# Kernel optimization log

Measured on AMD Instinct MI355X. Metric: run time of the kernel, lower is better.

Reference implementation:

```python
import jax, jax.numpy as jnp
import numpy as np

B, N, D, H = 32, 4096, 768, 384

def setup_inputs() -> dict:
    key = jax.random.key(0)
    k1, k2, k3 = jax.random.split(key, 3)
    patch_tokens = jax.random.normal(k1, (B, N, D), dtype=jnp.float32)
    # score head params (kaiming-like scale)
    w1 = jax.random.normal(k2, (D, H), dtype=jnp.float32) * (2.0 / H) ** 0.5
    b1 = jnp.zeros((H,), dtype=jnp.float32)
    w2 = jax.random.normal(k3, (H,), dtype=jnp.float32) * (2.0 / 1) ** 0.5
    b2 = jnp.zeros((), dtype=jnp.float32)
    return {"patch_tokens": patch_tokens, "w1": w1, "b1": b1, "w2": w2, "b2": b2,
            "keep_ratio_pct": 50}

def reference(patch_tokens, w1, b1, w2, b2, keep_ratio_pct):
    # score head: Linear -> GELU (erf variant, torch default) -> Linear(->1)
    h = jax.nn.gelu(jnp.einsum('bnd,dh->bnh', patch_tokens, w1) + b1, approximate=False)
    patch_logits = jnp.einsum('bnh,h->bn', h, w2) + b2                 # [B, N]
    foreground_scores = jax.nn.sigmoid(patch_logits)                    # [B, N]

    patch_count = patch_tokens.shape[1]
    keep_count = max(1, int(patch_count * keep_ratio_pct / 100))
    keep_count = min(keep_count, patch_count)

    if keep_count == patch_count:
        keep_mask = jnp.ones_like(foreground_scores)
    else:
        topk_scores, _ = jax.lax.top_k(foreground_scores, keep_count)   # [B, k], sorted desc
        keep_threshold = jax.lax.stop_gradient(topk_scores[:, -1:])     # [B, 1]
        keep_mask = (foreground_scores >= keep_threshold).astype(foreground_scores.dtype)

    filtered_scores = foreground_scores * keep_mask
    filtered_weights = filtered_scores / (jnp.sum(filtered_scores, axis=1, keepdims=True) + 1e-12)
    filtered_feat = jnp.einsum('bn,bnd->bd', filtered_weights, patch_tokens)  # [B, D]
    return (filtered_feat, filtered_weights, foreground_scores, keep_mask)
```

## Files before the change

kernel.cpp:

```cpp
#include <hip/hip_runtime.h>
#include <math.h>

#define BB 32
#define NN 4096
#define DD 768
#define HH 384
#define NCH 8

typedef _Float16 half8 __attribute__((ext_vector_type(8)));
typedef float f32x4 __attribute__((ext_vector_type(4)));

__global__ __launch_bounds__(64) void fapf_prep_w(
    const float* __restrict__ w1, short* __restrict__ whf, short* __restrict__ wlf)
{
    const int cf = blockIdx.x;
    const int kg = blockIdx.y;
    const int l  = threadIdx.x;
    const int c  = cf * 16 + (l & 15);
    const int kb = kg * 32 + (l >> 4) * 8;

    short hs[8], ls[8];
#pragma unroll
    for (int i = 0; i < 8; i++) {
        float v = w1[(size_t)(kb + i) * HH + c];
        _Float16 hi = (_Float16)v;
        _Float16 lo = (_Float16)(v - (float)hi);
        hs[i] = *(short*)&hi;
        ls[i] = *(short*)&lo;
    }
    size_t base = ((size_t)(kg * 24 + cf) * 64 + l) * 8;
#pragma unroll
    for (int i = 0; i < 8; i++) { whf[base + i] = hs[i]; wlf[base + i] = ls[i]; }
}

__global__ __launch_bounds__(256)
__attribute__((amdgpu_waves_per_eu(3)))
void fapf_scores_mfma(
    const float* __restrict__ x, const short* __restrict__ whf,
    const short* __restrict__ wlf, const float* __restrict__ b1,
    const float* __restrict__ w2, const float* __restrict__ b2,
    float* __restrict__ scores)
{
    __shared__ __align__(16) short xh[2][32 * 64];
    __shared__ __align__(16) short xl[2][32 * 64];
    __shared__ float part[32][4];

    const int tid = threadIdx.x;
    const int l   = tid & 63;
    const int cw  = tid >> 6;
    const int t0  = blockIdx.x * 32;

    f32x4 acc[2][6];
#pragma unroll
    for (int fr = 0; fr < 2; fr++)
#pragma unroll
        for (int cf = 0; cf < 6; cf++) acc[fr][cf] = (f32x4){0.f, 0.f, 0.f, 0.f};

    const half8* whp = (const half8*)whf + (size_t)(cw * 6) * 64 + l;
    const half8* wlp = (const half8*)wlf + (size_t)(cw * 6) * 64 + l;

    float4 xv[2];

#define LOADX(ch)                                                            \
    {                                                                        \
        _Pragma("unroll")                                                    \
        for (int it = 0; it < 2; it++) {                                     \
            int id = it * 256 + tid;                                         \
            xv[it] = *(const float4*)&x[(size_t)(t0 + (id >> 4)) * DD        \
                                        + (ch) * 64 + (id & 15) * 4];        \
        }                                                                    \
    }

#define SPLITWRITE(buf)                                                      \
    {                                                                        \
        _Pragma("unroll")                                                    \
        for (int it = 0; it < 2; it++) {                                     \
            int id = it * 256 + tid;                                         \
            int row = id >> 4, seg = id & 15;                                \
            union { short s[4]; uint2 u; } ph, pl;                           \
            float vv[4] = {xv[it].x, xv[it].y, xv[it].z, xv[it].w};          \
            _Pragma("unroll")                                                \
            for (int i = 0; i < 4; i++) {                                    \
                _Float16 hi = (_Float16)vv[i];                               \
                _Float16 lo = (_Float16)(vv[i] - (float)hi);                 \
                ph.s[i] = *(short*)&hi;                                      \
                pl.s[i] = *(short*)&lo;                                      \
            }                                                                \
            int idx = (row * 64 + seg * 4) ^ ((row & 7) << 3);               \
            *(uint2*)&xh[buf][idx] = ph.u;                                   \
            *(uint2*)&xl[buf][idx] = pl.u;                                   \
        }                                                                    \
    }

#define LOADB(dst, ptr, kg)                                                  \
    {                                                                        \
        _Pragma("unroll")                                                    \
        for (int cf = 0; cf < 6; cf++)                                       \
            dst[cf] = (ptr)[(size_t)(kg) * 1536 + (size_t)cf * 64];          \
    }

    LOADX(0);
    SPLITWRITE(0);
    half8 bA[6], bB[6];
    LOADB(bA, whp, 0);
    __syncthreads();

    for (int c = 0; c < 12; c++) {
        const int cur = c & 1;

#pragma unroll
        for (int ks = 0; ks < 2; ks++) {
            const int kg = c * 2 + ks;

            half8 ah[2], al[2];
#pragma unroll
            for (int fr = 0; fr < 2; fr++) {
                int row = fr * 16 + (l & 15);
                int idx = (row * 64 + ks * 32 + (l >> 4) * 8) ^ ((row & 7) << 3);
                ah[fr] = *(const half8*)&xh[cur][idx];
                al[fr] = *(const half8*)&xl[cur][idx];
            }

            LOADB(bB, wlp, kg);

            __builtin_amdgcn_s_setprio(1);
#pragma unroll
            for (int fr = 0; fr < 2; fr++)
#pragma unroll
                for (int cf = 0; cf < 6; cf++)
                    acc[fr][cf] = __builtin_amdgcn_mfma_f32_16x16x32_f16(
                        ah[fr], bA[cf], acc[fr][cf], 0, 0, 0);
#pragma unroll
            for (int fr = 0; fr < 2; fr++)
#pragma unroll
                for (int cf = 0; cf < 6; cf++)
                    acc[fr][cf] = __builtin_amdgcn_mfma_f32_16x16x32_f16(
                        al[fr], bA[cf], acc[fr][cf], 0, 0, 0);
            __builtin_amdgcn_s_setprio(0);

            if (kg < 23) LOADB(bA, whp, kg + 1);

            if (ks == 0 && c < 11) LOADX(c + 1);

            __builtin_amdgcn_s_setprio(1);
#pragma unroll
            for (int fr = 0; fr < 2; fr++)
#pragma unroll
                for (int cf = 0; cf < 6; cf++)
                    acc[fr][cf] = __builtin_amdgcn_mfma_f32_16x16x32_f16(
                        ah[fr], bB[cf], acc[fr][cf], 0, 0, 0);
            __builtin_amdgcn_s_setprio(0);
        }

        if (c < 11) {
            SPLITWRITE(cur ^ 1);
            __syncthreads();
        }
    }

    float b1v[6], w2v[6];
#pragma unroll
    for (int cf = 0; cf < 6; cf++) {
        int col = cw * 96 + cf * 16 + (l & 15);
        b1v[cf] = b1[col];
        w2v[cf] = w2[col];
    }
    float p[2][4];
#pragma unroll
    for (int fr = 0; fr < 2; fr++)
#pragma unroll
        for (int j = 0; j < 4; j++) p[fr][j] = 0.f;
#pragma unroll
    for (int fr = 0; fr < 2; fr++)
#pragma unroll
        for (int cf = 0; cf < 6; cf++)
#pragma unroll
            for (int j = 0; j < 4; j++) {
                float hh = acc[fr][cf][j] + b1v[cf];
                float g  = 0.5f * hh * (1.f + erff(hh * 0.70710678118654752f));
                p[fr][j] = fmaf(g, w2v[cf], p[fr][j]);
            }
#pragma unroll
    for (int m = 8; m >= 1; m >>= 1)
#pragma unroll
        for (int fr = 0; fr < 2; fr++)
#pragma unroll
            for (int j = 0; j < 4; j++)
                p[fr][j] += __shfl_xor(p[fr][j], m, 64);

    if ((l & 15) == 0) {
#pragma unroll
        for (int fr = 0; fr < 2; fr++)
#pragma unroll
            for (int j = 0; j < 4; j++) {
                int row = fr * 16 + (l >> 4) * 4 + j;
                part[row][cw] = p[fr][j];
            }
    }
    __syncthreads();
    if (tid < 32) {
        float lg = part[tid][0] + part[tid][1] + part[tid][2] + part[tid][3] + b2[0];
        scores[t0 + tid] = 1.f / (1.f + expf(-lg));
    }
#undef LOADX
#undef SPLITWRITE
#undef LOADB
}

__global__ __launch_bounds__(1024) void fapf_select_kernel(
    const float* __restrict__ scores, const int* __restrict__ pct_p,
    float* __restrict__ weights, float* __restrict__ mask,
    float* __restrict__ feat, int* __restrict__ kidx,
    float* __restrict__ kw, int* __restrict__ kcnt)
{
    __shared__ float s[NN];
    __shared__ float red[1024];
    __shared__ int scnt;
    const int b = blockIdx.x, tid = threadIdx.x;

    if (tid == 0) scnt = 0;
    for (int i = tid; i < DD; i += 1024) feat[b * DD + i] = 0.f;
    for (int i = tid; i < NN; i += 1024) s[i] = scores[b * NN + i];
    __syncthreads();

    for (int k = 2; k <= NN; k <<= 1) {
        for (int j = k >> 1; j > 0; j >>= 1) {
            for (int i = tid; i < NN; i += 1024) {
                int ixj = i ^ j;
                if (ixj > i) {
                    bool up = ((i & k) == 0);
                    float a = s[i], c = s[ixj];
                    if (up ? (a > c) : (a < c)) { s[i] = c; s[ixj] = a; }
                }
            }
            __syncthreads();
        }
    }

    int pct = pct_p[0];
    long long kcl = (long long)NN * pct / 100;
    int kc = (int)kcl;
    if (kc < 1) kc = 1;
    if (kc > NN) kc = NN;
    float thr = s[NN - kc];

    float local = 0.f;
    for (int i = tid; i < NN; i += 1024) {
        float v = scores[b * NN + i];
        if (v >= thr) local += v;
    }
    red[tid] = local;
    __syncthreads();
    for (int step = 512; step > 0; step >>= 1) {
        if (tid < step) red[tid] += red[tid + step];
        __syncthreads();
    }
    float inv = 1.f / (red[0] + 1e-12f);
    const int lane = tid & 63;
    for (int i = tid; i < NN; i += 1024) {
        float v = scores[b * NN + i];
        bool keep = (v >= thr);
        float m = keep ? 1.f : 0.f;
        weights[b * NN + i] = v * m * inv;
        mask[b * NN + i]    = m;
        if (kidx) {
            unsigned long long bal = __ballot(keep);
            int base = 0;
            if (lane == 0) base = atomicAdd(&scnt, __popcll(bal));
            base = __shfl(base, 0, 64);
            if (keep) {
                int off = __popcll(bal & ((1ULL << lane) - 1ULL));
                kidx[b * NN + base + off] = i;
                kw[b * NN + base + off]   = v * inv;
            }
        }
    }
    if (kidx) {
        __syncthreads();
        if (tid == 0) kcnt[b] = scnt;
    }
}

__global__ __launch_bounds__(256) void fapf_feat_compact(
    const float* __restrict__ x, const int* __restrict__ kidx,
    const float* __restrict__ kw, const int* __restrict__ kcnt,
    float* __restrict__ feat)
{
    const int b  = blockIdx.y;
    const int d0 = blockIdx.x * 64;
    const int ch = blockIdx.z;
    const int dl = threadIdx.x & 63;
    const int ng = threadIdx.x >> 6;

    const int cnt = kcnt[b];
    int per = (cnt + NCH - 1) / NCH;
    int j0 = ch * per; if (j0 > cnt) j0 = cnt;
    int j1 = j0 + per; if (j1 > cnt) j1 = cnt;
    int len = j1 - j0;
    int per_w = (len + 3) >> 2;
    int s = j0 + ng * per_w;
    int e = s + per_w; if (e > j1) e = j1;

    const float* xb  = x + (size_t)b * NN * DD + d0 + dl;
    const int*   ib  = kidx + b * NN;
    const float* wbp = kw + b * NN;

    float a[8];
#pragma unroll
    for (int u = 0; u < 8; u++) a[u] = 0.f;

    int j = s;
    for (; j + 8 <= e; j += 8) {
        int   idx[8];
        float ww[8];
#pragma unroll
        for (int u = 0; u < 8; u++) { idx[u] = ib[j + u]; ww[u] = wbp[j + u]; }
#pragma unroll
        for (int u = 0; u < 8; u++)
            a[u] = fmaf(ww[u], xb[(size_t)idx[u] * DD], a[u]);
    }
    for (; j < e; j++)
        a[0] = fmaf(wbp[j], xb[(size_t)ib[j] * DD], a[0]);

    float acc = ((a[0] + a[1]) + (a[2] + a[3])) + ((a[4] + a[5]) + (a[6] + a[7]));

    __shared__ float red[4][64];
    red[ng][dl] = acc;
    __syncthreads();
    if (threadIdx.x < 64) {
        float v = (red[0][dl] + red[1][dl]) + (red[2][dl] + red[3][dl]);
        atomicAdd(&feat[b * DD + d0 + dl], v);
    }
}

__global__ __launch_bounds__(256) void fapf_feat_dense(
    const float* __restrict__ x, const float* __restrict__ weights,
    float* __restrict__ feat)
{
    const int b  = blockIdx.y;
    const int d0 = blockIdx.x * 64;
    const int dl = threadIdx.x & 63;
    const int ng = threadIdx.x >> 6;

    const float* xb = x + (size_t)b * NN * DD;
    const float* wb = weights + b * NN;

    float a0 = 0.f, a1 = 0.f, a2 = 0.f, a3 = 0.f;
    for (int n = ng; n < NN; n += 16) {
        float w0 = wb[n], w1v = wb[n + 4], w2v = wb[n + 8], w3 = wb[n + 12];
        float v0 = xb[(size_t)(n)      * DD + d0 + dl];
        float v1 = xb[(size_t)(n + 4)  * DD + d0 + dl];
        float v2 = xb[(size_t)(n + 8)  * DD + d0 + dl];
        float v3 = xb[(size_t)(n + 12) * DD + d0 + dl];
        a0 = fmaf(w0, v0, a0);
        a1 = fmaf(w1v, v1, a1);
        a2 = fmaf(w2v, v2, a2);
        a3 = fmaf(w3, v3, a3);
    }
    float acc = (a0 + a1) + (a2 + a3);

    __shared__ float red[4][64];
    red[ng][dl] = acc;
    __syncthreads();
    if (threadIdx.x < 64) {
        feat[b * DD + d0 + dl] =
            (red[0][dl] + red[1][dl]) + (red[2][dl] + red[3][dl]);
    }
}

extern "C" void kernel_launch(void* const* d_in, const int* in_sizes, int n_in,
                              void* d_out, int out_size, void* d_ws, size_t ws_size,
                              hipStream_t stream) {
    const float* x   = (const float*)d_in[0];
    const float* w1  = (const float*)d_in[1];
    const float* b1  = (const float*)d_in[2];
    const float* w2  = (const float*)d_in[3];
    const float* b2  = (const float*)d_in[4];
    const int*   pct = (const int*)d_in[5];

    float* out = (float*)d_out;
    float* feat    = out;
    float* weights = out + BB * DD;
    float* scores  = weights + BB * NN;
    float* mask    = scores + BB * NN;

    short* whf  = (short*)d_ws;
    short* wlf  = whf + 24 * 24 * 64 * 8;
    int*   kidx = (int*)(wlf + 24 * 24 * 64 * 8);
    float* kw   = (float*)(kidx + BB * NN);
    int*   kcnt = (int*)(kw + BB * NN);

    const size_t needed = 2 * (size_t)(24 * 24 * 64 * 8) * sizeof(short)
                        + (size_t)BB * NN * (sizeof(int) + sizeof(float))
                        + BB * sizeof(int);
    const bool compact = ws_size >= needed;

    fapf_prep_w<<<dim3(24, 24), dim3(64), 0, stream>>>(w1, whf, wlf);
    fapf_scores_mfma<<<dim3(BB * NN / 32), dim3(256), 0, stream>>>(
        x, whf, wlf, b1, w2, b2, scores);
    fapf_select_kernel<<<dim3(BB), dim3(1024), 0, stream>>>(
        scores, pct, weights, mask, feat,
        compact ? kidx : (int*)nullptr, kw, kcnt);
    if (compact) {
        fapf_feat_compact<<<dim3(DD / 64, BB, NCH), dim3(256), 0, stream>>>(
            x, kidx, kw, kcnt, feat);
    } else {
        fapf_feat_dense<<<dim3(DD / 64, BB), dim3(256), 0, stream>>>(
            x, weights, feat);
    }
}
```

Before: 359.5 us.

## Replace bitonic sort with radix select and vectorize compact feature gather

```diff
diff --git a/kernel.cpp b/kernel.cpp
--- a/kernel.cpp
+++ b/kernel.cpp
@@ -139,7 +139,6 @@
             __builtin_amdgcn_s_setprio(0);
 
             if (kg < 23) LOADB(bA, whp, kg + 1);
-
             if (ks == 0 && c < 11) LOADX(c + 1);
 
             __builtin_amdgcn_s_setprio(1);
@@ -214,51 +213,87 @@
     float* __restrict__ kw, int* __restrict__ kcnt)
 {
     __shared__ float s[NN];
-    __shared__ float red[1024];
+    __shared__ unsigned int hist[256];
+    __shared__ unsigned int sh_bin, sh_above;
+    __shared__ float wsum[16];
     __shared__ int scnt;
     const int b = blockIdx.x, tid = threadIdx.x;
 
     if (tid == 0) scnt = 0;
     for (int i = tid; i < DD; i += 1024) feat[b * DD + i] = 0.f;
     for (int i = tid; i < NN; i += 1024) s[i] = scores[b * NN + i];
-    __syncthreads();
-
-    for (int k = 2; k <= NN; k <<= 1) {
-        for (int j = k >> 1; j > 0; j >>= 1) {
-            for (int i = tid; i < NN; i += 1024) {
-                int ixj = i ^ j;
-                if (ixj > i) {
-                    bool up = ((i & k) == 0);
-                    float a = s[i], c = s[ixj];
-                    if (up ? (a > c) : (a < c)) { s[i] = c; s[ixj] = a; }
-                }
-            }
-            __syncthreads();
-        }
-    }
 
     int pct = pct_p[0];
     long long kcl = (long long)NN * pct / 100;
     int kc = (int)kcl;
     if (kc < 1) kc = 1;
     if (kc > NN) kc = NN;
-    float thr = s[NN - kc];
+
+    __syncthreads();
+
+    unsigned int prefix = 0;
+    unsigned int kk = (unsigned int)kc;
+#pragma unroll
+    for (int pass = 0; pass < 4; pass++) {
+        const int shift = 24 - pass * 8;
+        if (tid < 256) hist[tid] = 0;
+        __syncthreads();
+        const unsigned int maskAbove =
+            (pass == 0) ? 0u : (0xFFFFFFFFu << (shift + 8));
+        for (int i = tid; i < NN; i += 1024) {
+            unsigned int u = __float_as_uint(s[i]);
+            if ((u & maskAbove) == prefix)
+                atomicAdd(&hist[(u >> shift) & 0xFFu], 1u);
+        }
+        __syncthreads();
+        if (tid < 64) {
+            const int ln = tid;
+            unsigned int h0 = hist[4 * ln + 0], h1 = hist[4 * ln + 1];
+            unsigned int h2 = hist[4 * ln + 2], h3 = hist[4 * ln + 3];
+            unsigned int lsum = h0 + h1 + h2 + h3;
+            unsigned int incl = lsum;
+#pragma unroll
+            for (int off = 1; off < 64; off <<= 1) {
+                unsigned int t = __shfl_down(incl, off, 64);
+                if (ln + off < 64) incl += t;
+            }
+            unsigned int above_lanes = incl - lsum;
+            unsigned int c3 = above_lanes + h3;
+            unsigned int c2 = c3 + h2;
+            unsigned int c1 = c2 + h1;
+            unsigned int c0 = c1 + h0;
+            if (c3 >= kk && above_lanes < kk) { sh_bin = 4u * ln + 3u; sh_above = above_lanes; }
+            if (c2 >= kk && c3 < kk)          { sh_bin = 4u * ln + 2u; sh_above = c3; }
+            if (c1 >= kk && c2 < kk)          { sh_bin = 4u * ln + 1u; sh_above = c2; }
+            if (c0 >= kk && c1 < kk)          { sh_bin = 4u * ln + 0u; sh_above = c1; }
+        }
+        __syncthreads();
+        kk -= sh_above;
+        prefix |= (sh_bin << shift);
+    }
+    const float thr = __uint_as_float(prefix);
 
     float local = 0.f;
     for (int i = tid; i < NN; i += 1024) {
-        float v = scores[b * NN + i];
+        float v = s[i];
         if (v >= thr) local += v;
     }
-    red[tid] = local;
-    __syncthreads();
-    for (int step = 512; step > 0; step >>= 1) {
-        if (tid < step) red[tid] += red[tid + step];
-        __syncthreads();
-    }
-    float inv = 1.f / (red[0] + 1e-12f);
+#pragma unroll
+    for (int off = 32; off >= 1; off >>= 1) local += __shfl_down(local, off, 64);
+    if ((tid & 63) == 0) wsum[tid >> 6] = local;
+    __syncthreads();
+    if (tid < 64) {
+        float t = (tid < 16) ? wsum[tid] : 0.f;
+#pragma unroll
+        for (int off = 8; off >= 1; off >>= 1) t += __shfl_down(t, off, 64);
+        if (tid == 0) wsum[0] = t;
+    }
+    __syncthreads();
+    const float inv = 1.f / (wsum[0] + 1e-12f);
+
     const int lane = tid & 63;
     for (int i = tid; i < NN; i += 1024) {
-        float v = scores[b * NN + i];
+        float v = s[i];
         bool keep = (v >= thr);
         float m = keep ? 1.f : 0.f;
         weights[b * NN + i] = v * m * inv;
@@ -287,7 +322,7 @@
     float* __restrict__ feat)
 {
     const int b  = blockIdx.y;
-    const int d0 = blockIdx.x * 64;
+    const int d0 = blockIdx.x * 256;
     const int ch = blockIdx.z;
     const int dl = threadIdx.x & 63;
     const int ng = threadIdx.x >> 6;
@@ -301,13 +336,13 @@
     int s = j0 + ng * per_w;
     int e = s + per_w; if (e > j1) e = j1;
 
-    const float* xb  = x + (size_t)b * NN * DD + d0 + dl;
+    const float* xb  = x + (size_t)b * NN * DD + d0 + dl * 4;
     const int*   ib  = kidx + b * NN;
     const float* wbp = kw + b * NN;
 
-    float a[8];
-#pragma unroll
-    for (int u = 0; u < 8; u++) a[u] = 0.f;
+    float4 a[8];
+#pragma unroll
+    for (int u = 0; u < 8; u++) a[u] = (float4){0.f, 0.f, 0.f, 0.f};
 
     int j = s;
     for (; j + 8 <= e; j += 8) {
@@ -315,21 +350,43 @@
         float ww[8];
 #pragma unroll
         for (int u = 0; u < 8; u++) { idx[u] = ib[j + u]; ww[u] = wbp[j + u]; }
+        float4 v[8];
 #pragma unroll
         for (int u = 0; u < 8; u++)
-            a[u] = fmaf(ww[u], xb[(size_t)idx[u] * DD], a[u]);
-    }
-    for (; j < e; j++)
-        a[0] = fmaf(wbp[j], xb[(size_t)ib[j] * DD], a[0]);
-
-    float acc = ((a[0] + a[1]) + (a[2] + a[3])) + ((a[4] + a[5]) + (a[6] + a[7]));
-
-    __shared__ float red[4][64];
+            v[u] = *(const float4*)&xb[(size_t)idx[u] * DD];
+#pragma unroll
+        for (int u = 0; u < 8; u++) {
+            a[u].x = fmaf(ww[u], v[u].x, a[u].x);
+            a[u].y = fmaf(ww[u], v[u].y, a[u].y);
+            a[u].z = fmaf(ww[u], v[u].z, a[u].z);
+            a[u].w = fmaf(ww[u], v[u].w, a[u].w);
+        }
+    }
+    for (; j < e; j++) {
+        float w = wbp[j];
+        float4 v = *(const float4*)&xb[(size_t)ib[j] * DD];
+        a[0].x = fmaf(w, v.x, a[0].x);
+        a[0].y = fmaf(w, v.y, a[0].y);
+        a[0].z = fmaf(w, v.z, a[0].z);
+        a[0].w = fmaf(w, v.w, a[0].w);
+    }
+
+    float4 acc;
+    acc.x = ((a[0].x + a[1].x) + (a[2].x + a[3].x)) + ((a[4].x + a[5].x) + (a[6].x + a[7].x));
+    acc.y = ((a[0].y + a[1].y) + (a[2].y + a[3].y)) + ((a[4].y + a[5].y) + (a[6].y + a[7].y));
+    acc.z = ((a[0].z + a[1].z) + (a[2].z + a[3].z)) + ((a[4].z + a[5].z) + (a[6].z + a[7].z));
+    acc.w = ((a[0].w + a[1].w) + (a[2].w + a[3].w)) + ((a[4].w + a[5].w) + (a[6].w + a[7].w));
+
+    __shared__ float4 red[4][64];
     red[ng][dl] = acc;
     __syncthreads();
     if (threadIdx.x < 64) {
-        float v = (red[0][dl] + red[1][dl]) + (red[2][dl] + red[3][dl]);
-        atomicAdd(&feat[b * DD + d0 + dl], v);
+        float4 r0 = red[0][dl], r1 = red[1][dl], r2 = red[2][dl], r3 = red[3][dl];
+        float* fp = &feat[b * DD + d0 + dl * 4];
+        atomicAdd(&fp[0], (r0.x + r1.x) + (r2.x + r3.x));
+        atomicAdd(&fp[1], (r0.y + r1.y) + (r2.y + r3.y));
+        atomicAdd(&fp[2], (r0.z + r1.z) + (r2.z + r3.z));
+        atomicAdd(&fp[3], (r0.w + r1.w) + (r2.w + r3.w));
     }
 }
 
@@ -402,7 +459,7 @@
         scores, pct, weights, mask, feat,
         compact ? kidx : (int*)nullptr, kw, kcnt);
     if (compact) {
-        fapf_feat_compact<<<dim3(DD / 64, BB, NCH), dim3(256), 0, stream>>>(
+        fapf_feat_compact<<<dim3(DD / 256, BB, NCH), dim3(256), 0, stream>>>(
             x, kidx, kw, kcnt, feat);
     } else {
         fapf_feat_dense<<<dim3(DD / 64, BB), dim3(256), 0, stream>>>(
```

After: 305.6 us (median of 2 runs). 1.18x faster.
